# Performance work log

Hardware: AMD Instinct MI355X
Metric: run time of the kernel (lower is better)

The kernel has to match this reference:

```python
import jax, jax.numpy as jnp
import numpy as np

# Grid constants (ERA5 0.25deg -> CESM ~1deg bilinear ESMF weights)
N_A = 721 * 1440      # 1,038,240 source cells
NY, NX = 192, 288
N_B = NY * NX         # 55,296 destination cells
NNZ = 4 * N_B         # ~4 weights per dst cell (bilinear)
LEAD = (2, 60)        # batch, channels


def setup_inputs() -> dict:
    key = jax.random.key(0)
    k1, k2, k3, k4 = jax.random.split(key, 4)
    x = jax.random.normal(k1, (*LEAD, 721, 1440), dtype=jnp.float32)
    weights = jax.random.uniform(k2, (NNZ,), dtype=jnp.float32)
    row = jax.random.randint(k3, (NNZ,), 0, N_B, dtype=jnp.int64)
    col = jax.random.randint(k4, (NNZ,), 0, N_A, dtype=jnp.int64)
    return {"x": x, "weights": weights, "row": row, "col": col}


def reference(x, weights, row, col):
    # torch.flip(x, dims=[-2]) : reverse latitude axis
    x = jnp.flip(x, axis=-2)
    lead_shape = x.shape[:-2]
    # x_flat: [M, n_a] where M = prod(lead dims)
    x_flat = x.reshape(-1, N_A)
    # Sparse W (n_b x n_a) @ x_flat.T as gather -> weight -> scatter-add:
    # gathered: [nnz, M]
    gathered = x_flat.T[col] * weights[:, None]
    # y: [n_b, M]
    y = jax.ops.segment_sum(gathered, row, num_segments=N_B)
    return y.T.reshape(*lead_shape, NY, NX)
```

## Files before the change

### kernel.cpp

```cpp
#include <hip/hip_runtime.h>
#include <stdint.h>

#define N_A     1038240
#define NXSRC   1440
#define NYSRC   721
#define N_B     55296
#define NNZ     221184
#define M_LEAD  120
#define CAP     32

#define NXCD        8
#define BLK         256
#define BBLKS       (N_B / BLK)
#define PLANES_XCD  (M_LEAD / NXCD)
#define WSCALE      4095.0f

__global__ void build_csr_kernel(const float* __restrict__ w,
                                 const int* __restrict__ row,
                                 const int* __restrict__ col,
                                 int* __restrict__ cnt,
                                 unsigned* __restrict__ entries) {
    int i = blockIdx.x * blockDim.x + threadIdx.x;
    if (i >= NNZ) return;
    int r = row[i];
    int c = col[i];
    int lat = c / NXSRC;
    int lon = c - lat * NXSRC;
    unsigned a = (unsigned)((NYSRC - 1 - lat) * NXSRC + lon);
    int wq = __float2int_rn(w[i] * WSCALE);
    wq = wq < 0 ? 0 : (wq > 4095 ? 4095 : wq);
    int pos = atomicAdd(&cnt[r], 1);
    if (pos < CAP) {
        entries[(size_t)pos * N_B + r] = (a << 12) | (unsigned)wq;
    }
}

__global__ void gather_kernel(const float* __restrict__ x,
                              const int* __restrict__ cnt,
                              const unsigned* __restrict__ entries,
                              float* __restrict__ out) {
    unsigned l    = blockIdx.x;
    unsigned xcd  = l & (NXCD - 1);
    unsigned slot = l >> 3;
    unsigned pix  = slot / BBLKS;
    unsigned bblk = slot - pix * BBLKS;
    unsigned m    = xcd * PLANES_XCD + pix;
    unsigned b    = bblk * BLK + threadIdx.x;

    const float* __restrict__ xm = x + (size_t)m * N_A;
    int n = cnt[b];
    if (n > CAP) n = CAP;
    float acc = 0.f;
    for (int k = 0; k < n; ++k) {
        unsigned e = entries[(size_t)k * N_B + b];
        acc += (float)(e & 0xFFFu) * xm[e >> 12];
    }
    __builtin_nontemporal_store(acc * (1.0f / WSCALE), &out[(size_t)m * N_B + b]);
}

__global__ void scatter_atomic_kernel(const float* __restrict__ x,
                                      const float* __restrict__ w,
                                      const int* __restrict__ row,
                                      const int* __restrict__ col,
                                      float* __restrict__ out) {
    int i = blockIdx.x * blockDim.x + threadIdx.x;
    if (i >= NNZ) return;
    int r = row[i];
    int c = col[i];
    int lat = c / NXSRC;
    int a   = (NYSRC - 1 - lat) * NXSRC + (c - lat * NXSRC);
    float wi = w[i];
    for (int m = 0; m < M_LEAD; ++m) {
        atomicAdd(&out[(size_t)m * N_B + r], wi * x[(size_t)m * N_A + a]);
    }
}

extern "C" void kernel_launch(void* const* d_in, const int* in_sizes, int n_in,
                              void* d_out, int out_size, void* d_ws, size_t ws_size,
                              hipStream_t stream) {
    const float* x   = (const float*)d_in[0];
    const float* w   = (const float*)d_in[1];
    const int*   row = (const int*)d_in[2];
    const int*   col = (const int*)d_in[3];
    float*       out = (float*)d_out;

    const size_t cnt_bytes     = (size_t)N_B * sizeof(int);
    const size_t entries_bytes = (size_t)CAP * N_B * sizeof(unsigned);
    const size_t need          = cnt_bytes + entries_bytes;

    if (ws_size >= need) {
        int*      cnt     = (int*)d_ws;
        unsigned* entries = (unsigned*)((char*)d_ws + cnt_bytes);

        hipMemsetAsync(cnt, 0, cnt_bytes, stream);
        build_csr_kernel<<<(NNZ + BLK - 1) / BLK, BLK, 0, stream>>>(w, row, col, cnt, entries);

        gather_kernel<<<BBLKS * M_LEAD, BLK, 0, stream>>>(x, cnt, entries, out);
    } else {
        hipMemsetAsync(out, 0, (size_t)M_LEAD * N_B * sizeof(float), stream);
        scatter_atomic_kernel<<<(NNZ + BLK - 1) / BLK, BLK, 0, stream>>>(x, w, row, col, out);
    }
}
```

Measured before the change: 263.1 us.

## Use fixed 8-slot row-major entry table with overflow list and atomic fixup

Replaces the column-major CAP=32 entry table with a per-row array of 8 packed entries, loaded as two uint4 vectors in a fully unrolled gather that has no data-dependent loop bound. Rows with more than 8 entries spill into an overflow list, which a separate fixup kernel applies with atomicAdd across all 120 planes. The goal is to cut per-thread loop overhead and make entry reads contiguous and vectorized. The cost is an extra kernel launch, a larger memset, and an overflow capacity of 8192 that silently drops entries beyond that count.

```diff
diff --git a/kernel.cpp b/kernel.cpp
--- a/kernel.cpp
+++ b/kernel.cpp
@@ -7,19 +7,29 @@
 #define N_B     55296
 #define NNZ     221184
 #define M_LEAD  120
-#define CAP     32
 
-#define NXCD        8
-#define BLK         256
-#define BBLKS       (N_B / BLK)
-#define PLANES_XCD  (M_LEAD / NXCD)
-#define WSCALE      4095.0f
+#define K1      8
+#define OVF_CAP 8192
+#define NXCD    8
+#define BLK     256
+#define BBLKS   (N_B / BLK)
+#define PLANES_XCD (M_LEAD / NXCD)
+#define WSCALE  4095.0f
 
-__global__ void build_csr_kernel(const float* __restrict__ w,
-                                 const int* __restrict__ row,
-                                 const int* __restrict__ col,
-                                 int* __restrict__ cnt,
-                                 unsigned* __restrict__ entries) {
+#define ENT8_OFF   0
+#define CNT_OFF    1769472
+#define OVFCNT_OFF 1990656
+#define OVF_OFF    1990672
+#define ZERO_BYTES 1990660
+#define WS_NEED    (OVF_OFF + OVF_CAP * 8)
+
+__global__ void build_kernel(const float* __restrict__ w,
+                             const int* __restrict__ row,
+                             const int* __restrict__ col,
+                             int* __restrict__ cnt,
+                             unsigned* __restrict__ ent8,
+                             int* __restrict__ ovf_cnt,
+                             uint2* __restrict__ ovf) {
     int i = blockIdx.x * blockDim.x + threadIdx.x;
     if (i >= NNZ) return;
     int r = row[i];
@@ -29,16 +39,19 @@
     unsigned a = (unsigned)((NYSRC - 1 - lat) * NXSRC + lon);
     int wq = __float2int_rn(w[i] * WSCALE);
     wq = wq < 0 ? 0 : (wq > 4095 ? 4095 : wq);
+    unsigned packed = (a << 12) | (unsigned)wq;
     int pos = atomicAdd(&cnt[r], 1);
-    if (pos < CAP) {
-        entries[(size_t)pos * N_B + r] = (a << 12) | (unsigned)wq;
+    if (pos < K1) {
+        ent8[r * K1 + pos] = packed;
+    } else {
+        int o = atomicAdd(ovf_cnt, 1);
+        if (o < OVF_CAP) ovf[o] = make_uint2((unsigned)r, packed);
     }
 }
 
-__global__ void gather_kernel(const float* __restrict__ x,
-                              const int* __restrict__ cnt,
-                              const unsigned* __restrict__ entries,
-                              float* __restrict__ out) {
+__global__ __launch_bounds__(BLK) void gather_kernel(const float* __restrict__ x,
+                                                     const uint4* __restrict__ ent4,
+                                                     float* __restrict__ out) {
     unsigned l    = blockIdx.x;
     unsigned xcd  = l & (NXCD - 1);
     unsigned slot = l >> 3;
@@ -48,14 +61,30 @@
     unsigned b    = bblk * BLK + threadIdx.x;
 
     const float* __restrict__ xm = x + (size_t)m * N_A;
-    int n = cnt[b];
-    if (n > CAP) n = CAP;
+    uint4 e0 = ent4[b * 2 + 0];
+    uint4 e1 = ent4[b * 2 + 1];
+    unsigned e[K1] = {e0.x, e0.y, e0.z, e0.w, e1.x, e1.y, e1.z, e1.w};
     float acc = 0.f;
-    for (int k = 0; k < n; ++k) {
-        unsigned e = entries[(size_t)k * N_B + b];
-        acc += (float)(e & 0xFFFu) * xm[e >> 12];
+#pragma unroll
+    for (int k = 0; k < K1; ++k) {
+        acc += (float)(e[k] & 0xFFFu) * xm[e[k] >> 12];
     }
     __builtin_nontemporal_store(acc * (1.0f / WSCALE), &out[(size_t)m * N_B + b]);
+}
+
+__global__ void fixup_kernel(const float* __restrict__ x,
+                             const int* __restrict__ ovf_cnt,
+                             const uint2* __restrict__ ovf,
+                             float* __restrict__ out) {
+    int t = blockIdx.x * blockDim.x + threadIdx.x;
+    int e_idx = t / M_LEAD;
+    int m = t - e_idx * M_LEAD;
+    int n = *ovf_cnt;
+    if (n > OVF_CAP) n = OVF_CAP;
+    if (e_idx >= n) return;
+    uint2 e = ovf[e_idx];
+    float wv = (float)(e.y & 0xFFFu) * (1.0f / WSCALE);
+    atomicAdd(&out[(size_t)m * N_B + e.x], wv * x[(size_t)m * N_A + (e.y >> 12)]);
 }
 
 __global__ void scatter_atomic_kernel(const float* __restrict__ x,
@@ -84,20 +113,24 @@
     const int*   col = (const int*)d_in[3];
     float*       out = (float*)d_out;
 
-    const size_t cnt_bytes     = (size_t)N_B * sizeof(int);
-    const size_t entries_bytes = (size_t)CAP * N_B * sizeof(unsigned);
-    const size_t need          = cnt_bytes + entries_bytes;
+    if (ws_size >= (size_t)WS_NEED) {
+        unsigned* ent8    = (unsigned*)((char*)d_ws + ENT8_OFF);
+        int*      cnt     = (int*)((char*)d_ws + CNT_OFF);
+        int*      ovf_cnt = (int*)((char*)d_ws + OVFCNT_OFF);
+        uint2*    ovf     = (uint2*)((char*)d_ws + OVF_OFF);
 
-    if (ws_size >= need) {
-        int*      cnt     = (int*)d_ws;
-        unsigned* entries = (unsigned*)((char*)d_ws + cnt_bytes);
+        hipMemsetAsync(d_ws, 0, ZERO_BYTES, stream);
+        build_kernel<<<(NNZ + BLK - 1) / BLK, BLK, 0, stream>>>(
+            w, row, col, cnt, ent8, ovf_cnt, ovf);
 
-        hipMemsetAsync(cnt, 0, cnt_bytes, stream);
-        build_csr_kernel<<<(NNZ + BLK - 1) / BLK, BLK, 0, stream>>>(w, row, col, cnt, entries);
+        gather_kernel<<<BBLKS * M_LEAD, BLK, 0, stream>>>(
+            x, (const uint4*)ent8, out);
 
-        gather_kernel<<<BBLKS * M_LEAD, BLK, 0, stream>>>(x, cnt, entries, out);
+        fixup_kernel<<<(OVF_CAP * M_LEAD + BLK - 1) / BLK, BLK, 0, stream>>>(
+            x, ovf_cnt, ovf, out);
     } else {
         hipMemsetAsync(out, 0, (size_t)M_LEAD * N_B * sizeof(float), stream);
-        scatter_atomic_kernel<<<(NNZ + BLK - 1) / BLK, BLK, 0, stream>>>(x, w, row, col, out);
+        scatter_atomic_kernel<<<(NNZ + BLK - 1) / BLK, BLK, 0, stream>>>(
+            x, w, row, col, out);
     }
 }
```

Result: no change. 260.3 us (-1.1%).
